# Kernel tuning notes

Measured on AMD Instinct MI355X. Metric: run time of the kernel, lower is better.

## Reference

```python
import jax, jax.numpy as jnp
import numpy as np

# NeuromorphicConfig defaults
DT = 1.0          # time_step
TAU = 20.0        # membrane_time_constant
THRESH = 1.0      # spike_threshold
RESET = 0.0       # reset_potential
REFRAC = 2.0      # refractory_period
SPARSE = 0.2      # sparse_connectivity
DECAY = float(np.exp(-DT / TAU))

I_SZ, H_SZ, O_SZ = 4096, 4096, 4096
T_STEPS = 128


def setup_inputs() -> dict:
    key = jax.random.key(0)
    ks = jax.random.split(key, 8)
    x = jax.random.uniform(ks[0], (I_SZ,), jnp.float32)          # rate-coded input in [0,1]
    u = jax.random.uniform(ks[1], (I_SZ,), jnp.float32)          # encoding noise (rand_like(x))
    W0 = jax.random.normal(ks[2], (H_SZ, I_SZ), jnp.float32) * 0.1
    W1 = jax.random.normal(ks[3], (H_SZ, H_SZ), jnp.float32) * 0.1
    W2 = jax.random.normal(ks[4], (O_SZ, H_SZ), jnp.float32) * 0.1
    M0 = (jax.random.uniform(ks[5], (H_SZ, I_SZ)) < SPARSE).astype(jnp.float32)
    M1 = (jax.random.uniform(ks[6], (H_SZ, H_SZ)) < SPARSE).astype(jnp.float32)
    M2 = (jax.random.uniform(ks[7], (O_SZ, H_SZ)) < SPARSE).astype(jnp.float32)
    return {"x": x, "u": u, "W0": W0, "W1": W1, "W2": W2,
            "M0": M0, "M1": M1, "M2": M2, "time_steps": T_STEPS}


def reference(x, u, W0, W1, W2, M0, M1, M2, time_steps):
    # effective (sparsity-masked) weights, fixed over time
    Ws = [W0 * M0, W1 * M1, W2 * M2]
    # rate coding: spikes at t=0 are (rand < x); zeros for t > 0
    enc = jnp.where(u < x, 1.0, 0.0).astype(x.dtype)
    inputs = jnp.zeros((time_steps, x.shape[0]), x.dtype).at[0].set(enc)  # [T, I]

    mems = tuple(jnp.zeros((W.shape[0],), x.dtype) for W in Ws)
    refs = tuple(jnp.zeros((W.shape[0],), x.dtype) for W in Ws)

    def step(carry, s):
        mems, refs = carry
        new_m, new_r = [], []
        for W, m, r in zip(Ws, mems, refs):
            cur = W @ s                                   # masked matvec [O]
            m = m * DECAY + cur                           # exp-decay integrate
            m = jnp.where(r > 0, RESET, m)                # clamp refractory neurons
            r = jnp.maximum(r - DT, 0.0)                  # refractory countdown
            spk = jnp.where(m > THRESH, 1.0, 0.0)         # threshold
            m = jnp.where(spk > 0, RESET, m)              # reset fired neurons
            r = jnp.where(spk > 0, REFRAC, r)             # enter refractory period
            new_m.append(m)
            new_r.append(r)
            s = spk                                       # feed spikes to next layer
        return (tuple(new_m), tuple(new_r)), s

    (_, _), out_spikes = jax.lax.scan(step, (mems, refs), inputs)  # out_spikes: [T, O]
    return out_spikes.mean(axis=0)  # rate-decoded output [O]
```

## Files before the change

### kernel.cpp

```cpp
#include <hip/hip_runtime.h>


constexpr int N = 4096;
typedef float f32x4 __attribute__((ext_vector_type(4)));

#define GLOBAL_AS __attribute__((address_space(1)))
#define LDS_AS    __attribute__((address_space(3)))

__global__ __launch_bounds__(256) void enc_kernel(
    const float* __restrict__ x, const float* __restrict__ u,
    unsigned long long* __restrict__ emask)
{
    const int j = blockIdx.x * 256 + threadIdx.x;
    const unsigned long long b = __ballot(u[j] < x[j]);
    if ((threadIdx.x & 63) == 0) emask[j >> 6] = b;
}

__device__ __forceinline__ void issue_chunk(
    const f32x4* __restrict__ Wrow, const f32x4* __restrict__ Mrow,
    int c, f32x4* ldsW, f32x4* ldsM, int lane)
{
#pragma unroll
    for (int i = 0; i < 4; ++i) {
        __builtin_amdgcn_global_load_lds(
            (const GLOBAL_AS void*)&Wrow[c * 256 + i * 64 + lane],
            (LDS_AS void*)&ldsW[i * 64], 16, 0, 0);
        __builtin_amdgcn_global_load_lds(
            (const GLOBAL_AS void*)&Mrow[c * 256 + i * 64 + lane],
            (LDS_AS void*)&ldsM[i * 64], 16, 0, 0);
    }
}

template <bool FINAL>
__global__ __launch_bounds__(256) void snn_layer(
    const float* __restrict__ W, const float* __restrict__ Mk,
    const unsigned int* __restrict__ in_mask,
    unsigned char* __restrict__ out_mask,
    const int* __restrict__ t_steps, float* __restrict__ out)
{
    const int lane = threadIdx.x & 63;
    const int wave = threadIdx.x >> 6;
    const int row0 = blockIdx.x * 8 + wave * 2;
    const int row1 = row0 + 1;

    __shared__ f32x4 sW[4][2][256];
    __shared__ f32x4 sM[4][2][256];
    __shared__ unsigned int smaskw[128];
    __shared__ int sbits[8];

    if (threadIdx.x < 128) smaskw[threadIdx.x] = in_mask[threadIdx.x];
    __syncthreads();
    const unsigned char* smb = (const unsigned char*)smaskw;

    const f32x4* Wr0 = reinterpret_cast<const f32x4*>(W  + (size_t)row0 * N);
    const f32x4* Wr1 = reinterpret_cast<const f32x4*>(W  + (size_t)row1 * N);
    const f32x4* Mr0 = reinterpret_cast<const f32x4*>(Mk + (size_t)row0 * N);
    const f32x4* Mr1 = reinterpret_cast<const f32x4*>(Mk + (size_t)row1 * N);

    issue_chunk(Wr0, Mr0, 0, &sW[wave][0][0], &sM[wave][0][0], lane);
    issue_chunk(Wr0, Mr0, 1, &sW[wave][1][0], &sM[wave][1][0], lane);

    double a0 = 0, a1 = 0, a2 = 0, a3 = 0;
    double b0 = 0, b1 = 0, b2 = 0, b3 = 0;

#define STEP(K, WN)                                                            \
    do {                                                                       \
        asm volatile("s_waitcnt vmcnt(" WN ")" ::: "memory");                  \
        __builtin_amdgcn_sched_barrier(0);                                     \
        const int c = (K) & 3;                                                 \
        const f32x4* bw = &sW[wave][(K) & 1][0];                               \
        const f32x4* bm = &sM[wave][(K) & 1][0];                               \
        f32x4 w[4], m[4];                                                      \
        unsigned int nb[4];                                                    \
        _Pragma("unroll")                                                      \
        for (int i = 0; i < 4; ++i) {                                          \
            w[i] = bw[i * 64 + lane];                                          \
            m[i] = bm[i * 64 + lane];                                          \
            const int idx = c * 256 + i * 64 + lane;                           \
            nb[i] = ((unsigned int)smb[idx >> 1] >> ((idx & 1) * 4)) & 0xFu;   \
        }                                                                      \
        asm volatile("s_waitcnt lgkmcnt(0)" ::: "memory");                     \
        __builtin_amdgcn_sched_barrier(0);                                     \
        if ((K) + 2 < 8)                                                       \
            issue_chunk(((K) + 2 < 4) ? Wr0 : Wr1, ((K) + 2 < 4) ? Mr0 : Mr1,  \
                        ((K) + 2) & 3, &sW[wave][(K) & 1][0],                  \
                        &sM[wave][(K) & 1][0], lane);                          \
        double& r0 = ((K) < 4) ? a0 : b0;                                      \
        double& r1 = ((K) < 4) ? a1 : b1;                                      \
        double& r2 = ((K) < 4) ? a2 : b2;                                      \
        double& r3 = ((K) < 4) ? a3 : b3;                                      \
        _Pragma("unroll")                                                      \
        for (int i = 0; i < 4; ++i) {                                          \
            r0 = fma((double)w[i].x, (double)((nb[i] & 1u) ? m[i].x : 0.0f), r0); \
            r1 = fma((double)w[i].y, (double)((nb[i] & 2u) ? m[i].y : 0.0f), r1); \
            r2 = fma((double)w[i].z, (double)((nb[i] & 4u) ? m[i].z : 0.0f), r2); \
            r3 = fma((double)w[i].w, (double)((nb[i] & 8u) ? m[i].w : 0.0f), r3); \
        }                                                                      \
    } while (0)

    STEP(0, "8"); STEP(1, "8"); STEP(2, "8"); STEP(3, "8");
    STEP(4, "8"); STEP(5, "8"); STEP(6, "8"); STEP(7, "0");
#undef STEP

    double t0 = (a0 + a1) + (a2 + a3);
    double t1 = (b0 + b1) + (b2 + b3);
#pragma unroll
    for (int off = 32; off > 0; off >>= 1) {
        t0 += __shfl_down(t0, off, 64);
        t1 += __shfl_down(t1, off, 64);
    }

    if (FINAL) {
        if (lane == 0) {
            const float sc = 1.0f / (float)t_steps[0];
            out[row0] = (t0 > 1.0) ? sc : 0.0f;
            out[row1] = (t1 > 1.0) ? sc : 0.0f;
        }
    } else {
        if (lane == 0) {
            sbits[2 * wave]     = (t0 > 1.0) ? 1 : 0;
            sbits[2 * wave + 1] = (t1 > 1.0) ? 1 : 0;
        }
        __syncthreads();
        if (threadIdx.x == 0) {
            unsigned int byte = 0;
#pragma unroll
            for (int i = 0; i < 8; ++i) byte |= (unsigned int)sbits[i] << i;
            out_mask[blockIdx.x] = (unsigned char)byte;
        }
    }
}

extern "C" void kernel_launch(void* const* d_in, const int* in_sizes, int n_in,
                              void* d_out, int out_size, void* d_ws, size_t ws_size,
                              hipStream_t stream)
{
    const float* x  = (const float*)d_in[0];
    const float* u  = (const float*)d_in[1];
    const float* W0 = (const float*)d_in[2];
    const float* W1 = (const float*)d_in[3];
    const float* W2 = (const float*)d_in[4];
    const float* M0 = (const float*)d_in[5];
    const float* M1 = (const float*)d_in[6];
    const float* M2 = (const float*)d_in[7];
    const int* t_steps = (const int*)d_in[8];
    float* out = (float*)d_out;

    unsigned long long* emask = (unsigned long long*)d_ws;
    unsigned char* m0 = (unsigned char*)d_ws + 512;
    unsigned char* m1 = (unsigned char*)d_ws + 1024;

    enc_kernel<<<dim3(16), dim3(256), 0, stream>>>(x, u, emask);
    snn_layer<false><<<dim3(512), dim3(256), 0, stream>>>(
        W0, M0, (const unsigned int*)emask, m0, nullptr, nullptr);
    snn_layer<false><<<dim3(512), dim3(256), 0, stream>>>(
        W1, M1, (const unsigned int*)m0, m1, nullptr, nullptr);
    snn_layer<true><<<dim3(512), dim3(256), 0, stream>>>(
        W2, M2, (const unsigned int*)m1, nullptr, t_steps, out);
}
```

Measured before the change: 344.9 us.

## Fuse three layer kernels into one persistent kernel with grid barriers

New measurement: 460.8 us. 1.34x slower.

```diff
diff --git a/kernel.cpp b/kernel.cpp
--- a/kernel.cpp
+++ b/kernel.cpp
@@ -2,6 +2,7 @@
 
 
 constexpr int N = 4096;
+constexpr int NBLOCKS = 512;
 typedef float f32x4 __attribute__((ext_vector_type(4)));
 
 #define GLOBAL_AS __attribute__((address_space(1)))
@@ -14,6 +15,20 @@
     const int j = blockIdx.x * 256 + threadIdx.x;
     const unsigned long long b = __ballot(u[j] < x[j]);
     if ((threadIdx.x & 63) == 0) emask[j >> 6] = b;
+}
+
+__device__ __forceinline__ void grid_barrier(int* cnt)
+{
+    __syncthreads();
+    if (threadIdx.x == 0) {
+        __threadfence();
+        atomicAdd(cnt, 1);
+        while (__hip_atomic_load(cnt, __ATOMIC_RELAXED,
+                                 __HIP_MEMORY_SCOPE_AGENT) < NBLOCKS)
+            __builtin_amdgcn_s_sleep(2);
+        __threadfence();
+    }
+    __syncthreads();
 }
 
 __device__ __forceinline__ void issue_chunk(
@@ -32,33 +47,26 @@
 }
 
 template <bool FINAL>
-__global__ __launch_bounds__(256) void snn_layer(
+__device__ __forceinline__ void snn_phase(
     const float* __restrict__ W, const float* __restrict__ Mk,
     const unsigned int* __restrict__ in_mask,
     unsigned char* __restrict__ out_mask,
-    const int* __restrict__ t_steps, float* __restrict__ out)
+    const int* __restrict__ t_steps, float* __restrict__ out,
+    f32x4* sWb, f32x4* sMb, unsigned int* smaskw, int* sbits,
+    int lane, int wave, int row0)
 {
-    const int lane = threadIdx.x & 63;
-    const int wave = threadIdx.x >> 6;
-    const int row0 = blockIdx.x * 8 + wave * 2;
-    const int row1 = row0 + 1;
-
-    __shared__ f32x4 sW[4][2][256];
-    __shared__ f32x4 sM[4][2][256];
-    __shared__ unsigned int smaskw[128];
-    __shared__ int sbits[8];
-
     if (threadIdx.x < 128) smaskw[threadIdx.x] = in_mask[threadIdx.x];
     __syncthreads();
     const unsigned char* smb = (const unsigned char*)smaskw;
 
+    const int row1 = row0 + 1;
     const f32x4* Wr0 = reinterpret_cast<const f32x4*>(W  + (size_t)row0 * N);
     const f32x4* Wr1 = reinterpret_cast<const f32x4*>(W  + (size_t)row1 * N);
     const f32x4* Mr0 = reinterpret_cast<const f32x4*>(Mk + (size_t)row0 * N);
     const f32x4* Mr1 = reinterpret_cast<const f32x4*>(Mk + (size_t)row1 * N);
 
-    issue_chunk(Wr0, Mr0, 0, &sW[wave][0][0], &sM[wave][0][0], lane);
-    issue_chunk(Wr0, Mr0, 1, &sW[wave][1][0], &sM[wave][1][0], lane);
+    issue_chunk(Wr0, Mr0, 0, sWb,       sMb,       lane);
+    issue_chunk(Wr0, Mr0, 1, sWb + 256, sMb + 256, lane);
 
     double a0 = 0, a1 = 0, a2 = 0, a3 = 0;
     double b0 = 0, b1 = 0, b2 = 0, b3 = 0;
@@ -68,8 +76,8 @@
         asm volatile("s_waitcnt vmcnt(" WN ")" ::: "memory");                  \
         __builtin_amdgcn_sched_barrier(0);                                     \
         const int c = (K) & 3;                                                 \
-        const f32x4* bw = &sW[wave][(K) & 1][0];                               \
-        const f32x4* bm = &sM[wave][(K) & 1][0];                               \
+        const f32x4* bw = sWb + ((K) & 1) * 256;                               \
+        const f32x4* bm = sMb + ((K) & 1) * 256;                               \
         f32x4 w[4], m[4];                                                      \
         unsigned int nb[4];                                                    \
         _Pragma("unroll")                                                      \
@@ -83,8 +91,8 @@
         __builtin_amdgcn_sched_barrier(0);                                     \
         if ((K) + 2 < 8)                                                       \
             issue_chunk(((K) + 2 < 4) ? Wr0 : Wr1, ((K) + 2 < 4) ? Mr0 : Mr1,  \
-                        ((K) + 2) & 3, &sW[wave][(K) & 1][0],                  \
-                        &sM[wave][(K) & 1][0], lane);                          \
+                        ((K) + 2) & 3, sWb + ((K) & 1) * 256,                  \
+                        sMb + ((K) & 1) * 256, lane);                          \
         double& r0 = ((K) < 4) ? a0 : b0;                                      \
         double& r1 = ((K) < 4) ? a1 : b1;                                      \
         double& r2 = ((K) < 4) ? a2 : b2;                                      \
@@ -131,6 +139,36 @@
     }
 }
 
+__global__ __launch_bounds__(256, 2) void snn_fused(
+    const float* __restrict__ W0, const float* __restrict__ W1,
+    const float* __restrict__ W2, const float* __restrict__ M0,
+    const float* __restrict__ M1, const float* __restrict__ M2,
+    const unsigned int* __restrict__ emask,
+    unsigned char* __restrict__ m0, unsigned char* __restrict__ m1,
+    const int* __restrict__ t_steps, float* __restrict__ out, int* bar)
+{
+    const int lane = threadIdx.x & 63;
+    const int wave = threadIdx.x >> 6;
+    const int row0 = blockIdx.x * 8 + wave * 2;
+
+    __shared__ f32x4 sW[4][2][256];
+    __shared__ f32x4 sM[4][2][256];
+    __shared__ unsigned int smaskw[128];
+    __shared__ int sbits[8];
+
+    snn_phase<false>(W0, M0, emask, m0, nullptr, nullptr,
+                     &sW[wave][0][0], &sM[wave][0][0], smaskw, sbits,
+                     lane, wave, row0);
+    grid_barrier(bar);
+    snn_phase<false>(W1, M1, (const unsigned int*)m0, m1, nullptr, nullptr,
+                     &sW[wave][0][0], &sM[wave][0][0], smaskw, sbits,
+                     lane, wave, row0);
+    grid_barrier(bar + 64);
+    snn_phase<true>(W2, M2, (const unsigned int*)m1, nullptr, t_steps, out,
+                    &sW[wave][0][0], &sM[wave][0][0], smaskw, sbits,
+                    lane, wave, row0);
+}
+
 extern "C" void kernel_launch(void* const* d_in, const int* in_sizes, int n_in,
                               void* d_out, int out_size, void* d_ws, size_t ws_size,
                               hipStream_t stream)
@@ -149,12 +187,12 @@
     unsigned long long* emask = (unsigned long long*)d_ws;
     unsigned char* m0 = (unsigned char*)d_ws + 512;
     unsigned char* m1 = (unsigned char*)d_ws + 1024;
+    int* bar = (int*)((unsigned char*)d_ws + 2048);
+
+    hipMemsetAsync(bar, 0, 128 * sizeof(int), stream);
 
     enc_kernel<<<dim3(16), dim3(256), 0, stream>>>(x, u, emask);
-    snn_layer<false><<<dim3(512), dim3(256), 0, stream>>>(
-        W0, M0, (const unsigned int*)emask, m0, nullptr, nullptr);
-    snn_layer<false><<<dim3(512), dim3(256), 0, stream>>>(
-        W1, M1, (const unsigned int*)m0, m1, nullptr, nullptr);
-    snn_layer<true><<<dim3(512), dim3(256), 0, stream>>>(
-        W2, M2, (const unsigned int*)m1, nullptr, t_steps, out);
+    snn_fused<<<dim3(NBLOCKS), dim3(256), 0, stream>>>(
+        W0, W1, W2, M0, M1, M2, (const unsigned int*)emask,
+        m0, m1, t_steps, out, bar);
 }
```
